# Kernel optimization log

Hardware: AMD Instinct MI355X
Metric: run time of the kernel (lower is better)

## Reference

```python
import jax, jax.numpy as jnp
import numpy as np

N, E, D, H, O = 100000, 1600000, 256, 128, 64


def setup_inputs() -> dict:
    key = jax.random.key(0)
    ks = jax.random.split(key, 10)
    x = jax.random.normal(ks[0], (N, D), dtype=jnp.float32)
    # edges without self loops (original adds remaining self loops itself)
    row = jax.random.randint(ks[1], (E,), 0, N)
    off = jax.random.randint(ks[2], (E,), 1, N)
    col = (row + off) % N
    edge_index = jnp.stack([row, col]).astype(jnp.int64)
    # positive PPMI edge weights (stand-in for cached random-walk PPMI values)
    ppmi_edge_weight = jax.random.uniform(ks[3], (E,), dtype=jnp.float32, minval=0.1, maxval=1.0)
    # glorot-style weights (shared between GCN and PPMI branches, as in the module)
    W1 = jax.random.normal(ks[4], (D, H), dtype=jnp.float32) * np.sqrt(2.0 / (D + H))
    b1 = jnp.zeros((H,), dtype=jnp.float32)
    W2 = jax.random.normal(ks[5], (H, O), dtype=jnp.float32) * np.sqrt(2.0 / (H + O))
    b2 = jnp.zeros((O,), dtype=jnp.float32)
    dense_w = jax.random.normal(ks[6], (O, 1), dtype=jnp.float32) * np.sqrt(2.0 / (O + 1))
    dense_b = jnp.zeros((1,), dtype=jnp.float32)
    return {"x": x, "edge_index": edge_index, "ppmi_edge_weight": ppmi_edge_weight,
            "W1": W1, "b1": b1, "W2": W2, "b2": b2,
            "dense_w": dense_w, "dense_b": dense_b}


def _sym_norm(row, col, ew, n):
    # deg^-0.5[row] * w * deg^-0.5[col], deg from scatter-add over source index
    deg = jax.ops.segment_sum(ew, row, num_segments=n)
    dis = jnp.where(deg > 0, deg ** -0.5, 0.0)
    return dis[row] * ew * dis[col]


def _gconv(h, W, b, row, col, norm, n):
    hw = h @ W                              # [N, F_out]
    msg = norm[:, None] * hw[row]           # gather + scale, [E', F_out]
    return jax.ops.segment_sum(msg, col, num_segments=n) + b


def reference(x, edge_index, ppmi_edge_weight, W1, b1, W2, b2, dense_w, dense_b):
    n = x.shape[0]
    row = edge_index[0].astype(jnp.int32)
    col = edge_index[1].astype(jnp.int32)
    sl = jnp.arange(n, dtype=jnp.int32)
    row_sl = jnp.concatenate([row, sl])
    col_sl = jnp.concatenate([col, sl])
    ones_sl = jnp.ones((n,), dtype=x.dtype)

    # GCN branch: edge_weight = 1, plus self loops (fill_value = 1)
    gcn_ew = jnp.concatenate([jnp.ones((row.shape[0],), dtype=x.dtype), ones_sl])
    gnorm = _sym_norm(row_sl, col_sl, gcn_ew, n)
    g = jax.nn.relu(_gconv(x, W1, b1, row_sl, col_sl, gnorm, n))  # dropout p in eval -> identity
    g = _gconv(g, W2, b2, row_sl, col_sl, gnorm, n)

    # PPMI branch: precomputed positive weights, plus self loops
    ppmi_ew = jnp.concatenate([ppmi_edge_weight.astype(x.dtype), ones_sl])
    pnorm = _sym_norm(row_sl, col_sl, ppmi_ew, n)
    p = jax.nn.relu(_gconv(x, W1, b1, row_sl, col_sl, pnorm, n))
    p = _gconv(p, W2, b2, row_sl, col_sl, pnorm, n)

    stacked = jnp.stack([g, p], axis=1)                 # [N, 2, O]
    logits = stacked @ dense_w + dense_b                # [N, 2, 1]
    w = jax.nn.softmax(logits, axis=1)
    return jnp.sum(stacked * w, axis=1)                 # [N, O]
```

## Files before the change

kernel.cpp:

```cpp
#include <hip/hip_runtime.h>
#include <hip/hip_bf16.h>
#include <math.h>

#define DD 256
#define HH 128
#define OO 64

#define EPB 8192
#define BKT 512

typedef __attribute__((ext_vector_type(8))) __bf16 bf16x8;
typedef __attribute__((ext_vector_type(4))) __bf16 bf16x4;
typedef __attribute__((ext_vector_type(4))) float f32x4;
typedef __attribute__((ext_vector_type(2))) float f32x2;

__device__ inline float2 bf2_to_f2(unsigned u) {
    float2 r;
    r.x = __uint_as_float(u << 16);
    r.y = __uint_as_float(u & 0xffff0000u);
    return r;
}

__global__ void part_count_kernel(const int* __restrict__ row, const int* __restrict__ col,
                                  int e, int nb,
                                  int* __restrict__ cnt_col, int* __restrict__ cnt_row) {
    __shared__ int hc[256], hr[256];
    int t = threadIdx.x;
    if (t < 256) { hc[t] = 0; hr[t] = 0; }
    __syncthreads();
    int base = blockIdx.x * EPB;
    int lim  = min(EPB, e - base);
    for (int i = t; i < lim; i += 512) {
        atomicAdd(&hc[col[base + i] >> 9], 1);
        atomicAdd(&hr[row[base + i] >> 9], 1);
    }
    __syncthreads();
    if (t < nb) {
        cnt_col[blockIdx.x * nb + t] = hc[t];
        cnt_row[blockIdx.x * nb + t] = hr[t];
    }
}

__global__ void scan_blocks_kernel(const int* __restrict__ cnt_col, const int* __restrict__ cnt_row,
                                   int* __restrict__ base_col, int* __restrict__ base_row,
                                   int* __restrict__ tot_col, int* __restrict__ tot_row,
                                   int nblk, int nb) {
    __shared__ int s[256];
    int side = (blockIdx.x >= (unsigned)nb) ? 1 : 0;
    int b = blockIdx.x - side * nb;
    const int* cnt = side ? cnt_row : cnt_col;
    int* base = side ? base_row : base_col;
    int* tot  = side ? tot_row  : tot_col;
    int t = threadIdx.x;
    int v = (t < nblk) ? cnt[(size_t)t * nb + b] : 0;
    s[t] = v;
    __syncthreads();
    for (int off = 1; off < 256; off <<= 1) {
        int u = (t >= off) ? s[t - off] : 0;
        __syncthreads();
        s[t] += u;
        __syncthreads();
    }
    if (t < nblk) base[(size_t)t * nb + b] = s[t] - v;
    if (t == 255) tot[b] = s[255];
}

__global__ void add_bases_kernel(int* __restrict__ base_col, int* __restrict__ base_row,
                                 const int* __restrict__ tot_col, const int* __restrict__ tot_row,
                                 int* __restrict__ bb_col, int* __restrict__ bb_row,
                                 int* __restrict__ row_ptr, int n, int e, int nblk, int nb) {
    __shared__ int s[256];
    __shared__ int bbv;
    int side = (blockIdx.x >= (unsigned)nb) ? 1 : 0;
    int b = blockIdx.x - side * nb;
    const int* tot = side ? tot_row : tot_col;
    int* base = side ? base_row : base_col;
    int t = threadIdx.x;
    int v = (t < nb) ? tot[t] : 0;
    s[t] = v;
    __syncthreads();
    for (int off = 1; off < 256; off <<= 1) {
        int u = (t >= off) ? s[t - off] : 0;
        __syncthreads();
        s[t] += u;
        __syncthreads();
    }
    if (t == 0) {
        bbv = (b > 0) ? s[b - 1] : 0;
        (side ? bb_row : bb_col)[b] = bbv;
    }
    __syncthreads();
    int add = bbv;
    for (int j = t; j < nblk; j += blockDim.x) base[(size_t)j * nb + b] += add;
    if (blockIdx.x == 0 && t == 0) row_ptr[n] = e;
}

__global__ void part_scatter_kernel(const int* __restrict__ row, const int* __restrict__ col,
                                    const float* __restrict__ ppmi,
                                    const int* __restrict__ base_col, const int* __restrict__ base_row,
                                    int4* __restrict__ tmp_col, int2* __restrict__ tmp_row,
                                    int e, int nb) {
    __shared__ int cc[256], cr[256];
    int t = threadIdx.x;
    if (t < nb) {
        cc[t] = base_col[blockIdx.x * nb + t];
        cr[t] = base_row[blockIdx.x * nb + t];
    }
    __syncthreads();
    int base = blockIdx.x * EPB;
    int lim  = min(EPB, e - base);
    for (int i = t; i < lim; i += 512) {
        int r = row[base + i], c = col[base + i];
        int w = __float_as_int(ppmi[base + i]);
        int sc = atomicAdd(&cc[c >> 9], 1);
        tmp_col[sc] = make_int4(c, r, w, 0);
        int sr = atomicAdd(&cr[r >> 9], 1);
        tmp_row[sr] = make_int2(r, w);
    }
}

__global__ void deg_bucket_kernel(const int2* __restrict__ tmp_row,
                                  const int* __restrict__ bb_row, const int* __restrict__ tot_row,
                                  float2* __restrict__ dis, int n) {
    __shared__ float dg[BKT], dp[BKT];
    int t = threadIdx.x;
    dg[t] = 1.0f; dp[t] = 1.0f;
    __syncthreads();
    int b = blockIdx.x;
    int beg = bb_row[b], cnt = tot_row[b];
    for (int i = t; i < cnt; i += 512) {
        int2 cell = tmp_row[beg + i];
        int lr = cell.x & (BKT - 1);
        atomicAdd(&dg[lr], 1.0f);
        atomicAdd(&dp[lr], __int_as_float(cell.y));
    }
    __syncthreads();
    int g = (b << 9) + t;
    if (g < n) dis[g] = make_float2(rsqrtf(dg[t]), rsqrtf(dp[t]));
}

__launch_bounds__(512)
__global__ void csr_bucket_kernel(const int4* __restrict__ tmp_col,
                                  const int* __restrict__ bb_col, const int* __restrict__ tot_col,
                                  const float2* __restrict__ dis,
                                  int* __restrict__ row_ptr, int4* __restrict__ csr_meta, int n) {
    __shared__ int hist[BKT], s[BKT], cur[BKT];
    int t = threadIdx.x;
    hist[t] = 0;
    __syncthreads();
    int b = blockIdx.x;
    int beg = bb_col[b], cnt = tot_col[b];
    for (int i = t; i < cnt; i += BKT) atomicAdd(&hist[tmp_col[beg + i].x & (BKT - 1)], 1);
    __syncthreads();
    int own = hist[t];
    s[t] = own;
    __syncthreads();
    for (int off = 1; off < BKT; off <<= 1) {
        int v = (t >= off) ? s[t - off] : 0;
        __syncthreads();
        s[t] += v;
        __syncthreads();
    }
    int gslot = beg + s[t] - own;
    cur[t] = gslot;
    int gc = (b << 9) + t;
    if (gc < n) row_ptr[gc] = gslot;
    __syncthreads();
    for (int i = t; i < cnt; i += BKT) {
        int4 cell = tmp_col[beg + i];
        int lc = cell.x & (BKT - 1);
        int slot = atomicAdd(&cur[lc], 1);
        int r = cell.y;
        float w = __int_as_float(cell.z);
        float2 d = dis[r];
        csr_meta[slot] = make_int4(r, __float_as_int(d.x), __float_as_int(d.y * w), 0);
    }
}

__global__ void conv_w_kernel(const float* __restrict__ W, __bf16* __restrict__ Bh,
                              __bf16* __restrict__ Bl, int K, int N) {
    int i = blockIdx.x * blockDim.x + threadIdx.x;
    if (i >= K * N) return;
    int k = i / N, nn = i % N;
    float v = W[i];
    __bf16 h = (__bf16)v;
    Bh[(size_t)nn * K + k] = h;
    Bl[(size_t)nn * K + k] = (__bf16)(v - (float)h);
}

template<int BNp, int K, bool ILV>
__launch_bounds__(512, 4)
__global__ void mfma_gemm_ldsb_kernel(const float* __restrict__ A,
                                      const __bf16* __restrict__ Bth, const __bf16* __restrict__ Btl,
                                      __bf16* __restrict__ C, int M, int nHalf,
                                      int ncg, int BNtot) {
    constexpr int NT  = BNp / 16;
    constexpr int GPC = K / 8;
    __shared__ __bf16 Bs[2][BNp][K];

    const int tid = threadIdx.x;
    const int cg  = blockIdx.x % ncg;
    const int rg  = blockIdx.x / ncg;
    const int cb  = cg * BNp;

    constexpr int TOT = 2 * BNp * GPC;
    for (int i = tid; i < TOT; i += 512) {
        int arr = i / (BNp * GPC);
        int rem = i - arr * (BNp * GPC);
        int c   = rem / GPC;
        int g   = rem - c * GPC;
        const __bf16* src = (arr ? Btl : Bth) + (size_t)(cb + c) * K + g * 8;
        uint4 v = *(const uint4*)src;
        *(uint4*)&Bs[arr][c][(g ^ (c & 7)) * 8] = v;
    }
    __syncthreads();

    const int wave = tid >> 6;
    const int lane = tid & 63;
    const int quad = lane >> 4;
    const int l16  = lane & 15;
    const int row0 = rg * 256 + wave * 32;
    if (row0 >= M) return;

    f32x4 acc[2][NT] = {};
    const float* ap0 = A + (size_t)(row0 + l16) * K + quad * 8;
    const float* ap1 = A + (size_t)(row0 + 16 + l16) * K + quad * 8;

    float4 a0[2][2];
    a0[0][0] = *(const float4*)ap0;  a0[0][1] = *(const float4*)(ap0 + 4);
    a0[1][0] = *(const float4*)ap1;  a0[1][1] = *(const float4*)(ap1 + 4);

    for (int k0 = 0; k0 < K; k0 += 32) {
        float4 a1[2][2];
        if (k0 + 32 < K) {
            a1[0][0] = *(const float4*)(ap0 + k0 + 32);
            a1[0][1] = *(const float4*)(ap0 + k0 + 36);
            a1[1][0] = *(const float4*)(ap1 + k0 + 32);
            a1[1][1] = *(const float4*)(ap1 + k0 + 36);
        }
        const int g0 = (k0 >> 3) + quad;
        bf16x8 bh[NT], bl[NT];
#pragma unroll
        for (int j = 0; j < NT; ++j) {
            int c  = j * 16 + l16;
            int gg = (g0 ^ (c & 7)) * 8;
            bh[j] = *(const bf16x8*)&Bs[0][c][gg];
            bl[j] = *(const bf16x8*)&Bs[1][c][gg];
        }
#pragma unroll
        for (int i = 0; i < 2; ++i) {
            float vv0 = a0[i][0].x, vv1 = a0[i][0].y, vv2 = a0[i][0].z, vv3 = a0[i][0].w;
            float vv4 = a0[i][1].x, vv5 = a0[i][1].y, vv6 = a0[i][1].z, vv7 = a0[i][1].w;
            __bf16 h0 = (__bf16)vv0, h1 = (__bf16)vv1, h2 = (__bf16)vv2, h3 = (__bf16)vv3;
            __bf16 h4 = (__bf16)vv4, h5 = (__bf16)vv5, h6 = (__bf16)vv6, h7 = (__bf16)vv7;
            bf16x8 ah = (bf16x8){h0, h1, h2, h3, h4, h5, h6, h7};
            bf16x8 al = (bf16x8){(__bf16)(vv0 - (float)h0), (__bf16)(vv1 - (float)h1),
                                 (__bf16)(vv2 - (float)h2), (__bf16)(vv3 - (float)h3),
                                 (__bf16)(vv4 - (float)h4), (__bf16)(vv5 - (float)h5),
                                 (__bf16)(vv6 - (float)h6), (__bf16)(vv7 - (float)h7)};
#pragma unroll
            for (int j = 0; j < NT; ++j) {
                acc[i][j] = __builtin_amdgcn_mfma_f32_16x16x32_bf16(ah, bh[j], acc[i][j], 0, 0, 0);
                acc[i][j] = __builtin_amdgcn_mfma_f32_16x16x32_bf16(ah, bl[j], acc[i][j], 0, 0, 0);
                acc[i][j] = __builtin_amdgcn_mfma_f32_16x16x32_bf16(al, bh[j], acc[i][j], 0, 0, 0);
            }
        }
        if (k0 + 32 < K) {
            a0[0][0] = a1[0][0]; a0[0][1] = a1[0][1];
            a0[1][0] = a1[1][0]; a0[1][1] = a1[1][1];
        }
    }

#pragma unroll
    for (int i = 0; i < 2; ++i) {
#pragma unroll
        for (int rg2 = 0; rg2 < 4; ++rg2) {
            int gr = row0 + i * 16 + quad * 4 + rg2;
            if constexpr (ILV) {
                int s = (gr >= nHalf) ? 1 : 0;
                size_t base = (size_t)(gr - s * nHalf) * (BNtot * 2) + s;
#pragma unroll
                for (int j = 0; j < NT; ++j)
                    C[base + (size_t)(cb + j * 16 + l16) * 2] = (__bf16)acc[i][j][rg2];
            } else {
#pragma unroll
                for (int j = 0; j < NT; ++j)
                    C[(size_t)gr * BNtot + cb + j * 16 + l16] = (__bf16)acc[i][j][rg2];
            }
        }
    }
}

__global__ void agg1_pull_kernel(const int* __restrict__ row_ptr, const int4* __restrict__ meta,
                                 const __bf16* __restrict__ hw1,
                                 const float2* __restrict__ dis,
                                 const float* __restrict__ b1,
                                 float* __restrict__ g_out, float* __restrict__ p_out, int n) {
    const int wave = threadIdx.x >> 6;
    const int lane = threadIdx.x & 63;
    int c = blockIdx.x * 4 + wave;
    if (c >= n) return;
    const int cu  = __builtin_amdgcn_readfirstlane(c);
    const int beg = __builtin_amdgcn_readfirstlane(row_ptr[cu]);
    const int end = __builtin_amdgcn_readfirstlane(row_ptr[cu + 1]);
    float sgx = 0.f, sgy = 0.f, spx = 0.f, spy = 0.f;
    int t = beg;
    for (; t + 8 <= end; t += 8) {
        int4 m[8];
#pragma unroll
        for (int q = 0; q < 8; ++q) m[q] = meta[t + q];
        unsigned u[8];
#pragma unroll
        for (int q = 0; q < 8; ++q) {
            const unsigned* rp = (const unsigned*)(hw1 + ((size_t)(unsigned)m[q].x << 7));
            u[q] = rp[lane];
        }
#pragma unroll
        for (int q = 0; q < 8; ++q) {
            float2 h = bf2_to_f2(u[q]);
            float wg = __uint_as_float((unsigned)m[q].y);
            float wp = __uint_as_float((unsigned)m[q].z);
            sgx += wg * h.x; sgy += wg * h.y;
            spx += wp * h.x; spy += wp * h.y;
        }
    }
    if (t + 4 <= end) {
        int4 m[4];
#pragma unroll
        for (int q = 0; q < 4; ++q) m[q] = meta[t + q];
        unsigned u[4];
#pragma unroll
        for (int q = 0; q < 4; ++q) {
            const unsigned* rp = (const unsigned*)(hw1 + ((size_t)(unsigned)m[q].x << 7));
            u[q] = rp[lane];
        }
#pragma unroll
        for (int q = 0; q < 4; ++q) {
            float2 h = bf2_to_f2(u[q]);
            float wg = __uint_as_float((unsigned)m[q].y);
            float wp = __uint_as_float((unsigned)m[q].z);
            sgx += wg * h.x; sgy += wg * h.y;
            spx += wp * h.x; spy += wp * h.y;
        }
        t += 4;
    }
    for (; t < end; ++t) {
        int4 m0 = meta[t];
        const unsigned* rp = (const unsigned*)(hw1 + ((size_t)(unsigned)m0.x << 7));
        float2 h0 = bf2_to_f2(rp[lane]);
        float wg0 = __uint_as_float((unsigned)m0.y);
        float wp0 = __uint_as_float((unsigned)m0.z);
        sgx += wg0 * h0.x; sgy += wg0 * h0.y;
        spx += wp0 * h0.x; spy += wp0 * h0.y;
    }

    const int f2 = lane * 2;
    float2 d = dis[c];
    size_t idx = ((size_t)c << 7) + f2;
    float2 hs = bf2_to_f2(*(const unsigned*)(hw1 + idx));
    float2 bv = *(const float2*)(b1 + f2);
    float gx = d.x * sgx + d.x * d.x * hs.x + bv.x;
    float gy = d.x * sgy + d.x * d.x * hs.y + bv.y;
    float px = d.y * spx + d.y * d.y * hs.x + bv.x;
    float py = d.y * spy + d.y * d.y * hs.y + bv.y;
    f32x2 go, po;
    go[0] = gx > 0.f ? gx : 0.f;  go[1] = gy > 0.f ? gy : 0.f;
    po[0] = px > 0.f ? px : 0.f;  po[1] = py > 0.f ? py : 0.f;
    __builtin_nontemporal_store(go, (f32x2*)(g_out + idx));
    __builtin_nontemporal_store(po, (f32x2*)(p_out + idx));
}

__global__ void agg2_final_kernel(const int* __restrict__ row_ptr, const int4* __restrict__ meta,
                                  const __bf16* __restrict__ hw2i,
                                  const float2* __restrict__ dis,
                                  const float* __restrict__ b2,
                                  const float* __restrict__ dense_w, const float* __restrict__ dense_b,
                                  float* __restrict__ out, int n) {
    const int wave = threadIdx.x >> 6;
    const int f    = threadIdx.x & 63;
    int c = blockIdx.x * 4 + wave;
    if (c >= n) return;
    const int cu  = __builtin_amdgcn_readfirstlane(c);
    const int beg = __builtin_amdgcn_readfirstlane(row_ptr[cu]);
    const int end = __builtin_amdgcn_readfirstlane(row_ptr[cu + 1]);
    float sg = 0.f, sp = 0.f;
    int t = beg;
    for (; t + 8 <= end; t += 8) {
        int4 m[8];
#pragma unroll
        for (int q = 0; q < 8; ++q) m[q] = meta[t + q];
        unsigned u[8];
#pragma unroll
        for (int q = 0; q < 8; ++q) {
            const unsigned* rp = (const unsigned*)(hw2i + ((size_t)(unsigned)m[q].x << 7));
            u[q] = rp[f];
        }
#pragma unroll
        for (int q = 0; q < 8; ++q) {
            float2 g0 = bf2_to_f2(u[q]);
            sg += __uint_as_float((unsigned)m[q].y) * g0.x;
            sp += __uint_as_float((unsigned)m[q].z) * g0.y;
        }
    }
    if (t + 4 <= end) {
        int4 m[4];
#pragma unroll
        for (int q = 0; q < 4; ++q) m[q] = meta[t + q];
        unsigned u[4];
#pragma unroll
        for (int q = 0; q < 4; ++q) {
            const unsigned* rp = (const unsigned*)(hw2i + ((size_t)(unsigned)m[q].x << 7));
            u[q] = rp[f];
        }
#pragma unroll
        for (int q = 0; q < 4; ++q) {
            float2 g0 = bf2_to_f2(u[q]);
            sg += __uint_as_float((unsigned)m[q].y) * g0.x;
            sp += __uint_as_float((unsigned)m[q].z) * g0.y;
        }
        t += 4;
    }
    for (; t < end; ++t) {
        int4 m0 = meta[t];
        const unsigned* rp = (const unsigned*)(hw2i + ((size_t)(unsigned)m0.x << 7));
        float2 g0 = bf2_to_f2(rp[f]);
        sg += __uint_as_float((unsigned)m0.y) * g0.x;
        sp += __uint_as_float((unsigned)m0.z) * g0.y;
    }

    const int f2 = f * 2;
    float2 d = dis[c];
    float2 gps = bf2_to_f2(*(const unsigned*)(hw2i + ((size_t)c << 7) + f2));
    float bb = b2[f];
    float gv = d.x * sg + d.x * d.x * gps.x + bb;
    float pv = d.y * sp + d.y * d.y * gps.y + bb;
    float dwv = dense_w[f];
    float lg = gv * dwv, lp = pv * dwv;
#pragma unroll
    for (int off = 32; off > 0; off >>= 1) {
        lg += __shfl_xor(lg, off, 64);
        lp += __shfl_xor(lp, off, 64);
    }
    lg += dense_b[0];
    lp += dense_b[0];
    float m  = fmaxf(lg, lp);
    float eg = expf(lg - m), ep = expf(lp - m);
    float wgt = eg / (eg + ep);
    __builtin_nontemporal_store(wgt * gv + (1.0f - wgt) * pv, out + (size_t)c * OO + f);
}

extern "C" void kernel_launch(void* const* d_in, const int* in_sizes, int n_in,
                              void* d_out, int out_size, void* d_ws, size_t ws_size,
                              hipStream_t stream) {
    const float* x    = (const float*)d_in[0];
    const int*   ei   = (const int*)d_in[1];
    const float* ppmi = (const float*)d_in[2];
    const float* W1   = (const float*)d_in[3];
    const float* b1   = (const float*)d_in[4];
    const float* W2   = (const float*)d_in[5];
    const float* b2   = (const float*)d_in[6];
    const float* dw   = (const float*)d_in[7];
    const float* db   = (const float*)d_in[8];
    float* out = (float*)d_out;

    const int n = in_sizes[0] / DD;
    const int e = in_sizes[2];
    const int* row = ei;
    const int* col = ei + e;

    const int nb   = (n + BKT - 1) / BKT;
    const int nblk = (e + EPB - 1) / EPB;

    float* ws      = (float*)d_ws;
    float2* dis    = (float2*)ws;
    __bf16* hw1    = (__bf16*)(ws + 2 * (size_t)n);
    float* g1      = (float*)(hw1 + (size_t)n * HH);
    float* p1      = g1 + (size_t)n * HH;
    int4* csr_meta = (int4*)(p1 + (size_t)n * HH);
    __bf16* bt1h   = (__bf16*)(csr_meta + e);
    __bf16* bt1l   = bt1h + (size_t)DD * HH;
    __bf16* bt2h   = bt1l + (size_t)DD * HH;
    __bf16* bt2l   = bt2h + (size_t)HH * OO;
    int* row_ptr   = (int*)(bt2l + (size_t)HH * OO);
    int* cnt_col   = row_ptr + (n + 1);
    int* base_col  = cnt_col + (size_t)nblk * nb;
    int* cnt_row   = base_col + (size_t)nblk * nb;
    int* base_row  = cnt_row + (size_t)nblk * nb;
    int* bb_col    = base_row + (size_t)nblk * nb;
    int* tot_col   = bb_col + nb;
    int* bb_row    = tot_col + nb;
    int* tot_row   = bb_row + nb;
    int4* tmp_col  = (int4*)g1;
    int2* tmp_row  = (int2*)p1;
    __bf16* hw2i   = hw1;

    const int T = 256;

    part_count_kernel<<<nblk, 512, 0, stream>>>(row, col, e, nb, cnt_col, cnt_row);
    scan_blocks_kernel<<<2 * nb, T, 0, stream>>>(cnt_col, cnt_row, base_col, base_row,
                                                 tot_col, tot_row, nblk, nb);
    add_bases_kernel<<<2 * nb, T, 0, stream>>>(base_col, base_row, tot_col, tot_row,
                                               bb_col, bb_row, row_ptr, n, e, nblk, nb);
    part_scatter_kernel<<<nblk, 512, 0, stream>>>(row, col, ppmi, base_col, base_row,
                                                  tmp_col, tmp_row, e, nb);
    deg_bucket_kernel<<<nb, 512, 0, stream>>>(tmp_row, bb_row, tot_row, dis, n);
    csr_bucket_kernel<<<nb, BKT, 0, stream>>>(tmp_col, bb_col, tot_col, dis,
                                              row_ptr, csr_meta, n);

    conv_w_kernel<<<(DD * HH + T - 1) / T, T, 0, stream>>>(W1, bt1h, bt1l, DD, HH);
    conv_w_kernel<<<(HH * OO + T - 1) / T, T, 0, stream>>>(W2, bt2h, bt2l, HH, OO);

    {
        int nrg = (n + 255) / 256;
        mfma_gemm_ldsb_kernel<64, 256, false><<<nrg * 2, 512, 0, stream>>>(
            x, bt1h, bt1l, hw1, n, 0, 2, HH);
    }
    agg1_pull_kernel<<<(n + 3) / 4, 256, 0, stream>>>(row_ptr, csr_meta, hw1, dis, b1, g1, p1, n);
    {
        int nrg = (2 * n + 255) / 256;
        mfma_gemm_ldsb_kernel<64, 128, true><<<nrg, 512, 0, stream>>>(
            g1, bt2h, bt2l, hw2i, 2 * n, n, 1, OO);
    }
    agg2_final_kernel<<<(n + 3) / 4, 256, 0, stream>>>(row_ptr, csr_meta, hw2i, dis,
                                                      b2, dw, db, out, n);
}
```

Baseline: 505.9 us.

## Compute degrees with global atomics instead of a row-bucketed partition pass

Drops the row-side partitioning (count, scan, scatter to tmp_row, and the per-bucket degree kernel). Degrees are now accumulated directly with global float atomicAdd from part_scatter into the dis buffer, which is initialised to 1 for the self loop and then passed through rsqrt in a small finalise kernel. The two weight-conversion launches are also merged into one. The aim is to cut memory traffic and launch count, at the cost of contended global atomics spread randomly over 100k nodes and non-deterministic float summation order.

Measured after the change: 599.3 us. 1.18x slower.

```diff
diff --git a/kernel.cpp b/kernel.cpp
--- a/kernel.cpp
+++ b/kernel.cpp
@@ -21,38 +21,32 @@
     return r;
 }
 
-__global__ void part_count_kernel(const int* __restrict__ row, const int* __restrict__ col,
-                                  int e, int nb,
-                                  int* __restrict__ cnt_col, int* __restrict__ cnt_row) {
-    __shared__ int hc[256], hr[256];
+__global__ void dis_init_kernel(float2* __restrict__ dis, int n) {
+    int i = blockIdx.x * blockDim.x + threadIdx.x;
+    if (i < n) dis[i] = make_float2(1.0f, 1.0f);
+}
+
+__global__ void part_count_kernel(const int* __restrict__ col,
+                                  int e, int nb, int* __restrict__ cnt_col) {
+    __shared__ int hc[256];
     int t = threadIdx.x;
-    if (t < 256) { hc[t] = 0; hr[t] = 0; }
+    if (t < 256) hc[t] = 0;
     __syncthreads();
     int base = blockIdx.x * EPB;
     int lim  = min(EPB, e - base);
-    for (int i = t; i < lim; i += 512) {
+    for (int i = t; i < lim; i += 512)
         atomicAdd(&hc[col[base + i] >> 9], 1);
-        atomicAdd(&hr[row[base + i] >> 9], 1);
-    }
-    __syncthreads();
-    if (t < nb) {
-        cnt_col[blockIdx.x * nb + t] = hc[t];
-        cnt_row[blockIdx.x * nb + t] = hr[t];
-    }
-}
-
-__global__ void scan_blocks_kernel(const int* __restrict__ cnt_col, const int* __restrict__ cnt_row,
-                                   int* __restrict__ base_col, int* __restrict__ base_row,
-                                   int* __restrict__ tot_col, int* __restrict__ tot_row,
+    __syncthreads();
+    if (t < nb) cnt_col[blockIdx.x * nb + t] = hc[t];
+}
+
+__global__ void scan_blocks_kernel(const int* __restrict__ cnt_col,
+                                   int* __restrict__ base_col, int* __restrict__ tot_col,
                                    int nblk, int nb) {
     __shared__ int s[256];
-    int side = (blockIdx.x >= (unsigned)nb) ? 1 : 0;
-    int b = blockIdx.x - side * nb;
-    const int* cnt = side ? cnt_row : cnt_col;
-    int* base = side ? base_row : base_col;
-    int* tot  = side ? tot_row  : tot_col;
+    int b = blockIdx.x;
     int t = threadIdx.x;
-    int v = (t < nblk) ? cnt[(size_t)t * nb + b] : 0;
+    int v = (t < nblk) ? cnt_col[(size_t)t * nb + b] : 0;
     s[t] = v;
     __syncthreads();
     for (int off = 1; off < 256; off <<= 1) {
@@ -61,22 +55,19 @@
         s[t] += u;
         __syncthreads();
     }
-    if (t < nblk) base[(size_t)t * nb + b] = s[t] - v;
-    if (t == 255) tot[b] = s[255];
-}
-
-__global__ void add_bases_kernel(int* __restrict__ base_col, int* __restrict__ base_row,
-                                 const int* __restrict__ tot_col, const int* __restrict__ tot_row,
-                                 int* __restrict__ bb_col, int* __restrict__ bb_row,
+    if (t < nblk) base_col[(size_t)t * nb + b] = s[t] - v;
+    if (t == 255) tot_col[b] = s[255];
+}
+
+__global__ void add_bases_kernel(int* __restrict__ base_col,
+                                 const int* __restrict__ tot_col,
+                                 int* __restrict__ bb_col,
                                  int* __restrict__ row_ptr, int n, int e, int nblk, int nb) {
     __shared__ int s[256];
     __shared__ int bbv;
-    int side = (blockIdx.x >= (unsigned)nb) ? 1 : 0;
-    int b = blockIdx.x - side * nb;
-    const int* tot = side ? tot_row : tot_col;
-    int* base = side ? base_row : base_col;
+    int b = blockIdx.x;
     int t = threadIdx.x;
-    int v = (t < nb) ? tot[t] : 0;
+    int v = (t < nb) ? tot_col[t] : 0;
     s[t] = v;
     __syncthreads();
     for (int off = 1; off < 256; off <<= 1) {
@@ -87,56 +78,42 @@
     }
     if (t == 0) {
         bbv = (b > 0) ? s[b - 1] : 0;
-        (side ? bb_row : bb_col)[b] = bbv;
+        bb_col[b] = bbv;
     }
     __syncthreads();
     int add = bbv;
-    for (int j = t; j < nblk; j += blockDim.x) base[(size_t)j * nb + b] += add;
+    for (int j = t; j < nblk; j += blockDim.x) base_col[(size_t)j * nb + b] += add;
     if (blockIdx.x == 0 && t == 0) row_ptr[n] = e;
 }
 
 __global__ void part_scatter_kernel(const int* __restrict__ row, const int* __restrict__ col,
                                     const float* __restrict__ ppmi,
-                                    const int* __restrict__ base_col, const int* __restrict__ base_row,
-                                    int4* __restrict__ tmp_col, int2* __restrict__ tmp_row,
+                                    const int* __restrict__ base_col,
+                                    int4* __restrict__ tmp_col,
+                                    float* __restrict__ deg,
                                     int e, int nb) {
-    __shared__ int cc[256], cr[256];
+    __shared__ int cc[256];
     int t = threadIdx.x;
-    if (t < nb) {
-        cc[t] = base_col[blockIdx.x * nb + t];
-        cr[t] = base_row[blockIdx.x * nb + t];
-    }
+    if (t < nb) cc[t] = base_col[blockIdx.x * nb + t];
     __syncthreads();
     int base = blockIdx.x * EPB;
     int lim  = min(EPB, e - base);
     for (int i = t; i < lim; i += 512) {
         int r = row[base + i], c = col[base + i];
-        int w = __float_as_int(ppmi[base + i]);
+        float wf = ppmi[base + i];
         int sc = atomicAdd(&cc[c >> 9], 1);
-        tmp_col[sc] = make_int4(c, r, w, 0);
-        int sr = atomicAdd(&cr[r >> 9], 1);
-        tmp_row[sr] = make_int2(r, w);
-    }
-}
-
-__global__ void deg_bucket_kernel(const int2* __restrict__ tmp_row,
-                                  const int* __restrict__ bb_row, const int* __restrict__ tot_row,
-                                  float2* __restrict__ dis, int n) {
-    __shared__ float dg[BKT], dp[BKT];
-    int t = threadIdx.x;
-    dg[t] = 1.0f; dp[t] = 1.0f;
-    __syncthreads();
-    int b = blockIdx.x;
-    int beg = bb_row[b], cnt = tot_row[b];
-    for (int i = t; i < cnt; i += 512) {
-        int2 cell = tmp_row[beg + i];
-        int lr = cell.x & (BKT - 1);
-        atomicAdd(&dg[lr], 1.0f);
-        atomicAdd(&dp[lr], __int_as_float(cell.y));
-    }
-    __syncthreads();
-    int g = (b << 9) + t;
-    if (g < n) dis[g] = make_float2(rsqrtf(dg[t]), rsqrtf(dp[t]));
+        tmp_col[sc] = make_int4(c, r, __float_as_int(wf), 0);
+        atomicAdd(deg + 2 * (size_t)r, 1.0f);
+        atomicAdd(deg + 2 * (size_t)r + 1, wf);
+    }
+}
+
+__global__ void dis_fin_kernel(float2* __restrict__ dis, int n) {
+    int i = blockIdx.x * blockDim.x + threadIdx.x;
+    if (i < n) {
+        float2 d = dis[i];
+        dis[i] = make_float2(rsqrtf(d.x), rsqrtf(d.y));
+    }
 }
 
 __launch_bounds__(512)
@@ -177,15 +154,25 @@
     }
 }
 
-__global__ void conv_w_kernel(const float* __restrict__ W, __bf16* __restrict__ Bh,
-                              __bf16* __restrict__ Bl, int K, int N) {
+__global__ void conv_w_kernel(const float* __restrict__ W1, __bf16* __restrict__ B1h,
+                              __bf16* __restrict__ B1l,
+                              const float* __restrict__ W2, __bf16* __restrict__ B2h,
+                              __bf16* __restrict__ B2l) {
     int i = blockIdx.x * blockDim.x + threadIdx.x;
-    if (i >= K * N) return;
-    int k = i / N, nn = i % N;
-    float v = W[i];
-    __bf16 h = (__bf16)v;
-    Bh[(size_t)nn * K + k] = h;
-    Bl[(size_t)nn * K + k] = (__bf16)(v - (float)h);
+    if (i < DD * HH) {
+        int k = i / HH, nn = i % HH;
+        float v = W1[i];
+        __bf16 h = (__bf16)v;
+        B1h[(size_t)nn * DD + k] = h;
+        B1l[(size_t)nn * DD + k] = (__bf16)(v - (float)h);
+    } else if (i < DD * HH + HH * OO) {
+        int j = i - DD * HH;
+        int k = j / OO, nn = j % OO;
+        float v = W2[j];
+        __bf16 h = (__bf16)v;
+        B2h[(size_t)nn * HH + k] = h;
+        B2l[(size_t)nn * HH + k] = (__bf16)(v - (float)h);
+    }
 }
 
 template<int BNp, int K, bool ILV>
@@ -484,31 +471,25 @@
     int* row_ptr   = (int*)(bt2l + (size_t)HH * OO);
     int* cnt_col   = row_ptr + (n + 1);
     int* base_col  = cnt_col + (size_t)nblk * nb;
-    int* cnt_row   = base_col + (size_t)nblk * nb;
-    int* base_row  = cnt_row + (size_t)nblk * nb;
-    int* bb_col    = base_row + (size_t)nblk * nb;
+    int* bb_col    = base_col + (size_t)nblk * nb;
     int* tot_col   = bb_col + nb;
-    int* bb_row    = tot_col + nb;
-    int* tot_row   = bb_row + nb;
     int4* tmp_col  = (int4*)g1;
-    int2* tmp_row  = (int2*)p1;
     __bf16* hw2i   = hw1;
 
     const int T = 256;
 
-    part_count_kernel<<<nblk, 512, 0, stream>>>(row, col, e, nb, cnt_col, cnt_row);
-    scan_blocks_kernel<<<2 * nb, T, 0, stream>>>(cnt_col, cnt_row, base_col, base_row,
-                                                 tot_col, tot_row, nblk, nb);
-    add_bases_kernel<<<2 * nb, T, 0, stream>>>(base_col, base_row, tot_col, tot_row,
-                                               bb_col, bb_row, row_ptr, n, e, nblk, nb);
-    part_scatter_kernel<<<nblk, 512, 0, stream>>>(row, col, ppmi, base_col, base_row,
-                                                  tmp_col, tmp_row, e, nb);
-    deg_bucket_kernel<<<nb, 512, 0, stream>>>(tmp_row, bb_row, tot_row, dis, n);
+    dis_init_kernel<<<(n + 1023) / 1024, 1024, 0, stream>>>(dis, n);
+    part_count_kernel<<<nblk, 512, 0, stream>>>(col, e, nb, cnt_col);
+    scan_blocks_kernel<<<nb, T, 0, stream>>>(cnt_col, base_col, tot_col, nblk, nb);
+    add_bases_kernel<<<nb, T, 0, stream>>>(base_col, tot_col, bb_col, row_ptr, n, e, nblk, nb);
+    part_scatter_kernel<<<nblk, 512, 0, stream>>>(row, col, ppmi, base_col,
+                                                  tmp_col, (float*)dis, e, nb);
+    dis_fin_kernel<<<(n + 1023) / 1024, 1024, 0, stream>>>(dis, n);
     csr_bucket_kernel<<<nb, BKT, 0, stream>>>(tmp_col, bb_col, tot_col, dis,
                                               row_ptr, csr_meta, n);
 
-    conv_w_kernel<<<(DD * HH + T - 1) / T, T, 0, stream>>>(W1, bt1h, bt1l, DD, HH);
-    conv_w_kernel<<<(HH * OO + T - 1) / T, T, 0, stream>>>(W2, bt2h, bt2l, HH, OO);
+    conv_w_kernel<<<(DD * HH + HH * OO + T - 1) / T, T, 0, stream>>>(W1, bt1h, bt1l,
+                                                                     W2, bt2h, bt2l);
 
     {
         int nrg = (n + 255) / 256;
```
